# Optimization experiments

Measured on AMD Instinct MI355X. Metric: run time of the kernel, lower is better.

The kernel has to match this reference:

```python
import jax, jax.numpy as jnp
import numpy as np

B, H, E = 1024, 2048, 1024

def _xavier(key, shape):
    # torch xavier_normal_ on [1, out, in]: std = sqrt(2/(fan_in+fan_out)) over last two dims
    fan_out, fan_in = shape[-2], shape[-1]
    std = (2.0 / (fan_in + fan_out)) ** 0.5
    return jax.random.normal(key, shape, jnp.float32) * std

def setup_inputs() -> dict:
    key = jax.random.key(0)
    ks = jax.random.split(key, 17)
    inp = {
        'x': jax.random.normal(ks[0], (B, E, 1), jnp.float32),
        'c': jax.random.normal(ks[1], (B, H, 1), jnp.float32),
        'h': jax.random.normal(ks[2], (B, H, 1), jnp.float32),
        'W_xi': _xavier(ks[3], (1, H, E)), 'W_hi': _xavier(ks[4], (1, H, H)), 'B_i': _xavier(ks[5], (1, H, 1)),
        'W_xg': _xavier(ks[6], (1, H, E)), 'W_hg': _xavier(ks[7], (1, H, H)), 'B_g': _xavier(ks[8], (1, H, 1)),
        'W_xf': _xavier(ks[9], (1, H, E)), 'W_hf': _xavier(ks[10], (1, H, H)), 'B_f': _xavier(ks[11], (1, H, 1)),
        'W_xo': _xavier(ks[12], (1, H, E)), 'W_ho': _xavier(ks[13], (1, H, H)), 'B_o': _xavier(ks[14], (1, H, 1)),
        'W_hy': _xavier(ks[15], (1, E, H)), 'B_y': _xavier(ks[16], (1, E, 1)),
    }
    return inp

def reference(x, c, h, W_xi, W_hi, B_i, W_xg, W_hg, B_g, W_xf, W_hf, B_f, W_xo, W_ho, B_o, W_hy, B_y):
    # jnp.matmul broadcasts the leading batch dim: [1,H,E] @ [B,E,1] -> [B,H,1]
    i = jax.nn.sigmoid(jnp.matmul(W_xi, x) + jnp.matmul(W_hi, h) + B_i)
    g = jnp.tanh(jnp.matmul(W_xg, x) + jnp.matmul(W_hg, h) + B_g)
    f = jax.nn.sigmoid(jnp.matmul(W_xf, x) + jnp.matmul(W_hf, h) + B_f)
    c_new = f * c + i * g
    o = jax.nn.sigmoid(jnp.matmul(W_xo, x) + jnp.matmul(W_ho, h) + B_o)
    h_new = o * c_new  # NOTE: source uses o*c (no tanh), faithful to original
    y = jnp.tanh(jnp.matmul(W_hy, h_new) + B_y)
    return (y, c_new, h_new)
```

## Files before the change

### kernel.cpp

```cpp
#include <hip/hip_runtime.h>

#define B_SZ 1024
#define H_SZ 2048
#define E_SZ 1024

typedef float  f32x4 __attribute__((ext_vector_type(4)));
typedef short  s16x8 __attribute__((ext_vector_type(8)));

__device__ __forceinline__ unsigned short f2bf(float f) {
    unsigned u = __float_as_uint(f);
    u = u + 0x7fffu + ((u >> 16) & 1u);
    return (unsigned short)(u >> 16);
}
__device__ __forceinline__ float bf2f(unsigned short s) {
    return __uint_as_float(((unsigned)s) << 16);
}

struct CastArgs {
    const float*    src[11];
    unsigned short* dst[11];
    int             n[11];
};

__global__ __launch_bounds__(256) void cast_kernel(CastArgs a) {
    const int arr = blockIdx.y;
    const int n = a.n[arr];
    const float* __restrict__ s = a.src[arr];
    unsigned short* __restrict__ d = a.dst[arr];
    const int stride = gridDim.x * 256 * 4;
    for (int i = (blockIdx.x * 256 + threadIdx.x) * 4; i < n; i += stride) {
        float4 v = *(const float4*)(s + i);
        ushort4 o;
        o.x = f2bf(v.x); o.y = f2bf(v.y); o.z = f2bf(v.z); o.w = f2bf(v.w);
        *(ushort4*)(d + i) = o;
    }
}

__device__ __forceinline__ void gemm_accum(
    const unsigned short* __restrict__ A,
    const unsigned short* __restrict__ W,
    int K, int m0, int n0,
    unsigned short* lA, unsigned short* lB,
    f32x4 acc[4][4], int t)
{
    const int lane = t & 63;
    const int w    = t >> 6;
    const int wr   = (w >> 1) << 6;
    const int wc   = (w & 1) << 6;
    const int lr   = lane & 15;
    const int kq   = (lane >> 4) << 3;

    const int r0   = t >> 2;
    const int col0 = (t & 3) << 3;

    for (int k0 = 0; k0 < K; k0 += 32) {
        const unsigned short* ga0 = A + (size_t)(m0 + r0) * K + (k0 + col0);
        const unsigned short* ga1 = ga0 + (size_t)64 * K;
        const unsigned short* gb0 = W + (size_t)(n0 + r0) * K + (k0 + col0);
        const unsigned short* gb1 = gb0 + (size_t)64 * K;
        __builtin_amdgcn_global_load_lds(
            (const __attribute__((address_space(1))) unsigned int*)ga0,
            (__attribute__((address_space(3))) unsigned int*)(lA + t * 8), 16, 0, 0);
        __builtin_amdgcn_global_load_lds(
            (const __attribute__((address_space(1))) unsigned int*)ga1,
            (__attribute__((address_space(3))) unsigned int*)(lA + (t + 256) * 8), 16, 0, 0);
        __builtin_amdgcn_global_load_lds(
            (const __attribute__((address_space(1))) unsigned int*)gb0,
            (__attribute__((address_space(3))) unsigned int*)(lB + t * 8), 16, 0, 0);
        __builtin_amdgcn_global_load_lds(
            (const __attribute__((address_space(1))) unsigned int*)gb1,
            (__attribute__((address_space(3))) unsigned int*)(lB + (t + 256) * 8), 16, 0, 0);
        __syncthreads();

        s16x8 af[4], bfr[4];
#pragma unroll
        for (int i = 0; i < 4; ++i)
            af[i] = *(const s16x8*)(lA + (wr + i * 16 + lr) * 32 + kq);
#pragma unroll
        for (int j = 0; j < 4; ++j)
            bfr[j] = *(const s16x8*)(lB + (wc + j * 16 + lr) * 32 + kq);
#pragma unroll
        for (int i = 0; i < 4; ++i)
#pragma unroll
            for (int j = 0; j < 4; ++j)
                acc[i][j] = __builtin_amdgcn_mfma_f32_16x16x32_bf16(
                    af[i], bfr[j], acc[i][j], 0, 0, 0);
        __syncthreads();
    }
}

__global__ __launch_bounds__(256) void gates_kernel(
    const unsigned short* __restrict__ Xb,
    const unsigned short* __restrict__ Hb,
    const unsigned short* __restrict__ Wxb,
    const unsigned short* __restrict__ Whb,
    const float* __restrict__ bi, const float* __restrict__ bg,
    const float* __restrict__ bff, const float* __restrict__ bo,
    unsigned short* __restrict__ Z)
{
    __shared__ unsigned short lA[128 * 32];
    __shared__ unsigned short lB[128 * 32];
    const int t  = threadIdx.x;
    const int m0 = blockIdx.x * 128;
    const int q  = blockIdx.y >> 4;
    const int n0 = (blockIdx.y & 15) * 128;

    f32x4 acc[4][4] = {};
    gemm_accum(Xb, Wxb + (size_t)q * H_SZ * E_SZ, E_SZ, m0, n0, lA, lB, acc, t);
    gemm_accum(Hb, Whb + (size_t)q * H_SZ * H_SZ, H_SZ, m0, n0, lA, lB, acc, t);

    const float* bias = (q == 0) ? bi : (q == 1) ? bg : (q == 2) ? bff : bo;
    const int lane = t & 63, w = t >> 6;
    const int wr = (w >> 1) << 6, wc = (w & 1) << 6;
    const int lr = lane & 15, rq = (lane >> 4) << 2;
    unsigned short* Zq = Z + (size_t)q * B_SZ * H_SZ;
#pragma unroll
    for (int i = 0; i < 4; ++i) {
#pragma unroll
        for (int j = 0; j < 4; ++j) {
            const int n = n0 + wc + j * 16 + lr;
            const float bv = bias[n];
#pragma unroll
            for (int r = 0; r < 4; ++r) {
                const int m = m0 + wr + i * 16 + rq + r;
                const float v = acc[i][j][r] + bv;
                const float a = (q == 1) ? tanhf(v) : 1.0f / (1.0f + __expf(-v));
                Zq[(size_t)m * H_SZ + n] = f2bf(a);
            }
        }
    }
}

__global__ __launch_bounds__(256) void cell_kernel(
    const unsigned short* __restrict__ Z, const float* __restrict__ c,
    float* __restrict__ c_out, float* __restrict__ h_out,
    unsigned short* __restrict__ HnB)
{
    const size_t BH = (size_t)B_SZ * H_SZ;
    const int idx = (blockIdx.x * 256 + threadIdx.x) * 4;
    ushort4 iu = *(const ushort4*)(Z + idx);
    ushort4 gu = *(const ushort4*)(Z + BH + idx);
    ushort4 fu = *(const ushort4*)(Z + 2 * BH + idx);
    ushort4 ou = *(const ushort4*)(Z + 3 * BH + idx);
    float4 cv = *(const float4*)(c + idx);

    float cn[4], hn[4];
    cn[0] = bf2f(fu.x) * cv.x + bf2f(iu.x) * bf2f(gu.x);
    cn[1] = bf2f(fu.y) * cv.y + bf2f(iu.y) * bf2f(gu.y);
    cn[2] = bf2f(fu.z) * cv.z + bf2f(iu.z) * bf2f(gu.z);
    cn[3] = bf2f(fu.w) * cv.w + bf2f(iu.w) * bf2f(gu.w);
    hn[0] = bf2f(ou.x) * cn[0];
    hn[1] = bf2f(ou.y) * cn[1];
    hn[2] = bf2f(ou.z) * cn[2];
    hn[3] = bf2f(ou.w) * cn[3];

    *(float4*)(c_out + idx) = make_float4(cn[0], cn[1], cn[2], cn[3]);
    *(float4*)(h_out + idx) = make_float4(hn[0], hn[1], hn[2], hn[3]);
    ushort4 hb;
    hb.x = f2bf(hn[0]); hb.y = f2bf(hn[1]); hb.z = f2bf(hn[2]); hb.w = f2bf(hn[3]);
    *(ushort4*)(HnB + idx) = hb;
}

__global__ __launch_bounds__(256) void y_kernel(
    const unsigned short* __restrict__ Hn,
    const unsigned short* __restrict__ Wy,
    const float* __restrict__ by, float* __restrict__ yout)
{
    __shared__ unsigned short lA[128 * 32];
    __shared__ unsigned short lB[128 * 32];
    const int t  = threadIdx.x;
    const int m0 = blockIdx.x * 128;
    const int n0 = blockIdx.y * 128;

    f32x4 acc[4][4] = {};
    gemm_accum(Hn, Wy, H_SZ, m0, n0, lA, lB, acc, t);

    const int lane = t & 63, w = t >> 6;
    const int wr = (w >> 1) << 6, wc = (w & 1) << 6;
    const int lr = lane & 15, rq = (lane >> 4) << 2;
#pragma unroll
    for (int i = 0; i < 4; ++i) {
#pragma unroll
        for (int j = 0; j < 4; ++j) {
            const int n = n0 + wc + j * 16 + lr;
            const float bv = by[n];
#pragma unroll
            for (int r = 0; r < 4; ++r) {
                const int m = m0 + wr + i * 16 + rq + r;
                yout[(size_t)m * E_SZ + n] = tanhf(acc[i][j][r] + bv);
            }
        }
    }
}

extern "C" void kernel_launch(void* const* d_in, const int* in_sizes, int n_in,
                              void* d_out, int out_size, void* d_ws, size_t ws_size,
                              hipStream_t stream) {
    const float* x   = (const float*)d_in[0];
    const float* c   = (const float*)d_in[1];
    const float* h   = (const float*)d_in[2];
    const float* Wxi = (const float*)d_in[3];
    const float* Whi = (const float*)d_in[4];
    const float* Bi  = (const float*)d_in[5];
    const float* Wxg = (const float*)d_in[6];
    const float* Whg = (const float*)d_in[7];
    const float* Bg  = (const float*)d_in[8];
    const float* Wxf = (const float*)d_in[9];
    const float* Whf = (const float*)d_in[10];
    const float* Bf  = (const float*)d_in[11];
    const float* Wxo = (const float*)d_in[12];
    const float* Who = (const float*)d_in[13];
    const float* Bo  = (const float*)d_in[14];
    const float* Why = (const float*)d_in[15];
    const float* By  = (const float*)d_in[16];

    const size_t BE = (size_t)B_SZ * E_SZ, BH = (size_t)B_SZ * H_SZ;
    const size_t HE = (size_t)H_SZ * E_SZ, HH = (size_t)H_SZ * H_SZ;
    const size_t EH = (size_t)E_SZ * H_SZ;

    unsigned short* ws   = (unsigned short*)d_ws;
    unsigned short* Xb   = ws;
    unsigned short* Hb   = Xb + BE;
    unsigned short* Wxb  = Hb + BH;
    unsigned short* Whb  = Wxb + 4 * HE;
    unsigned short* Whyb = Whb + 4 * HH;
    unsigned short* Z    = Whyb + EH;
    unsigned short* HnB  = Z + 4 * BH;

    CastArgs ca;
    ca.src[0]  = x;   ca.dst[0]  = Xb;           ca.n[0]  = (int)BE;
    ca.src[1]  = h;   ca.dst[1]  = Hb;           ca.n[1]  = (int)BH;
    ca.src[2]  = Wxi; ca.dst[2]  = Wxb;          ca.n[2]  = (int)HE;
    ca.src[3]  = Wxg; ca.dst[3]  = Wxb + HE;     ca.n[3]  = (int)HE;
    ca.src[4]  = Wxf; ca.dst[4]  = Wxb + 2 * HE; ca.n[4]  = (int)HE;
    ca.src[5]  = Wxo; ca.dst[5]  = Wxb + 3 * HE; ca.n[5]  = (int)HE;
    ca.src[6]  = Whi; ca.dst[6]  = Whb;          ca.n[6]  = (int)HH;
    ca.src[7]  = Whg; ca.dst[7]  = Whb + HH;     ca.n[7]  = (int)HH;
    ca.src[8]  = Whf; ca.dst[8]  = Whb + 2 * HH; ca.n[8]  = (int)HH;
    ca.src[9]  = Who; ca.dst[9]  = Whb + 3 * HH; ca.n[9]  = (int)HH;
    ca.src[10] = Why; ca.dst[10] = Whyb;         ca.n[10] = (int)EH;

    hipLaunchKernelGGL(cast_kernel, dim3(1024, 11), dim3(256), 0, stream, ca);
    hipLaunchKernelGGL(gates_kernel, dim3(8, 64), dim3(256), 0, stream,
                       Xb, Hb, Wxb, Whb, Bi, Bg, Bf, Bo, Z);

    float* y_out = (float*)d_out;
    float* c_out = y_out + BE;
    float* h_out = c_out + BH;
    hipLaunchKernelGGL(cell_kernel, dim3((unsigned)(BH / 1024)), dim3(256), 0, stream,
                       Z, c, c_out, h_out, HnB);
    hipLaunchKernelGGL(y_kernel, dim3(8, 8), dim3(256), 0, stream,
                       HnB, Whyb, By, y_out);
}
```

Measured before the change: 309.2 us.

## Split-K the output GEMM and remap gate tiles for XCD-local weight reuse

The y GEMM was launched on only 64 blocks. It is now split four ways along K into 256 blocks that write fp32 partials into the reused Z buffer, and a separate reduce kernel sums the partials and applies bias and tanh. The gates kernel moves to a 1D grid whose block index is remapped so blocks on the same XCD share weight N-tiles, aiming for better L2 locality. The split adds an extra kernel launch and partial-sum traffic to memory.

```diff
diff --git a/kernel.cpp b/kernel.cpp
--- a/kernel.cpp
+++ b/kernel.cpp
@@ -39,7 +39,7 @@
 __device__ __forceinline__ void gemm_accum(
     const unsigned short* __restrict__ A,
     const unsigned short* __restrict__ W,
-    int K, int m0, int n0,
+    int ld, int kLen, int m0, int n0,
     unsigned short* lA, unsigned short* lB,
     f32x4 acc[4][4], int t)
 {
@@ -53,11 +53,11 @@
     const int r0   = t >> 2;
     const int col0 = (t & 3) << 3;
 
-    for (int k0 = 0; k0 < K; k0 += 32) {
-        const unsigned short* ga0 = A + (size_t)(m0 + r0) * K + (k0 + col0);
-        const unsigned short* ga1 = ga0 + (size_t)64 * K;
-        const unsigned short* gb0 = W + (size_t)(n0 + r0) * K + (k0 + col0);
-        const unsigned short* gb1 = gb0 + (size_t)64 * K;
+    for (int k0 = 0; k0 < kLen; k0 += 32) {
+        const unsigned short* ga0 = A + (size_t)(m0 + r0) * ld + (k0 + col0);
+        const unsigned short* ga1 = ga0 + (size_t)64 * ld;
+        const unsigned short* gb0 = W + (size_t)(n0 + r0) * ld + (k0 + col0);
+        const unsigned short* gb1 = gb0 + (size_t)64 * ld;
         __builtin_amdgcn_global_load_lds(
             (const __attribute__((address_space(1))) unsigned int*)ga0,
             (__attribute__((address_space(3))) unsigned int*)(lA + t * 8), 16, 0, 0);
@@ -100,14 +100,18 @@
 {
     __shared__ unsigned short lA[128 * 32];
     __shared__ unsigned short lB[128 * 32];
-    const int t  = threadIdx.x;
-    const int m0 = blockIdx.x * 128;
-    const int q  = blockIdx.y >> 4;
-    const int n0 = (blockIdx.y & 15) * 128;
+    const int t   = threadIdx.x;
+    const int b   = blockIdx.x;
+    const int xcd = b & 7;
+    const int i_  = b >> 3;
+    const int nt  = xcd * 8 + (i_ >> 3);
+    const int m0  = (i_ & 7) * 128;
+    const int q   = nt >> 4;
+    const int n0  = (nt & 15) * 128;
 
     f32x4 acc[4][4] = {};
-    gemm_accum(Xb, Wxb + (size_t)q * H_SZ * E_SZ, E_SZ, m0, n0, lA, lB, acc, t);
-    gemm_accum(Hb, Whb + (size_t)q * H_SZ * H_SZ, H_SZ, m0, n0, lA, lB, acc, t);
+    gemm_accum(Xb, Wxb + (size_t)q * H_SZ * E_SZ, E_SZ, E_SZ, m0, n0, lA, lB, acc, t);
+    gemm_accum(Hb, Whb + (size_t)q * H_SZ * H_SZ, H_SZ, H_SZ, m0, n0, lA, lB, acc, t);
 
     const float* bias = (q == 0) ? bi : (q == 1) ? bg : (q == 2) ? bff : bo;
     const int lane = t & 63, w = t >> 6;
@@ -161,36 +165,61 @@
     *(ushort4*)(HnB + idx) = hb;
 }
 
-__global__ __launch_bounds__(256) void y_kernel(
+__global__ __launch_bounds__(256) void y_split_kernel(
     const unsigned short* __restrict__ Hn,
     const unsigned short* __restrict__ Wy,
-    const float* __restrict__ by, float* __restrict__ yout)
+    float* __restrict__ part)
 {
     __shared__ unsigned short lA[128 * 32];
     __shared__ unsigned short lB[128 * 32];
-    const int t  = threadIdx.x;
-    const int m0 = blockIdx.x * 128;
-    const int n0 = blockIdx.y * 128;
+    const int t   = threadIdx.x;
+    const int b   = blockIdx.x;
+    const int xcd = b & 7;
+    const int i_  = b >> 3;
+    const int ns  = xcd * 4 + (i_ >> 3);
+    const int m0  = (i_ & 7) * 128;
+    const int n0  = (ns >> 2) * 128;
+    const int s   = ns & 3;
 
     f32x4 acc[4][4] = {};
-    gemm_accum(Hn, Wy, H_SZ, m0, n0, lA, lB, acc, t);
+    gemm_accum(Hn + s * 512, Wy + s * 512, H_SZ, 512, m0, n0, lA, lB, acc, t);
 
     const int lane = t & 63, w = t >> 6;
     const int wr = (w >> 1) << 6, wc = (w & 1) << 6;
     const int lr = lane & 15, rq = (lane >> 4) << 2;
+    float* P = part + (size_t)s * B_SZ * E_SZ;
 #pragma unroll
     for (int i = 0; i < 4; ++i) {
 #pragma unroll
         for (int j = 0; j < 4; ++j) {
             const int n = n0 + wc + j * 16 + lr;
-            const float bv = by[n];
 #pragma unroll
             for (int r = 0; r < 4; ++r) {
                 const int m = m0 + wr + i * 16 + rq + r;
-                yout[(size_t)m * E_SZ + n] = tanhf(acc[i][j][r] + bv);
+                P[(size_t)m * E_SZ + n] = acc[i][j][r];
             }
         }
     }
+}
+
+__global__ __launch_bounds__(256) void y_reduce_kernel(
+    const float* __restrict__ part, const float* __restrict__ by,
+    float* __restrict__ yout)
+{
+    const size_t BE = (size_t)B_SZ * E_SZ;
+    const int idx = (blockIdx.x * 256 + threadIdx.x) * 4;
+    float4 a = *(const float4*)(part + idx);
+    float4 b2 = *(const float4*)(part + BE + idx);
+    float4 c2 = *(const float4*)(part + 2 * BE + idx);
+    float4 d2 = *(const float4*)(part + 3 * BE + idx);
+    const int col = idx & (E_SZ - 1);
+    float4 bv = *(const float4*)(by + col);
+    float4 o;
+    o.x = tanhf(a.x + b2.x + c2.x + d2.x + bv.x);
+    o.y = tanhf(a.y + b2.y + c2.y + d2.y + bv.y);
+    o.z = tanhf(a.z + b2.z + c2.z + d2.z + bv.z);
+    o.w = tanhf(a.w + b2.w + c2.w + d2.w + bv.w);
+    *(float4*)(yout + idx) = o;
 }
 
 extern "C" void kernel_launch(void* const* d_in, const int* in_sizes, int n_in,
@@ -241,7 +270,7 @@
     ca.src[10] = Why; ca.dst[10] = Whyb;         ca.n[10] = (int)EH;
 
     hipLaunchKernelGGL(cast_kernel, dim3(1024, 11), dim3(256), 0, stream, ca);
-    hipLaunchKernelGGL(gates_kernel, dim3(8, 64), dim3(256), 0, stream,
+    hipLaunchKernelGGL(gates_kernel, dim3(512), dim3(256), 0, stream,
                        Xb, Hb, Wxb, Whb, Bi, Bg, Bf, Bo, Z);
 
     float* y_out = (float*)d_out;
@@ -249,6 +278,10 @@
     float* h_out = c_out + BH;
     hipLaunchKernelGGL(cell_kernel, dim3((unsigned)(BH / 1024)), dim3(256), 0, stream,
                        Z, c, c_out, h_out, HnB);
-    hipLaunchKernelGGL(y_kernel, dim3(8, 8), dim3(256), 0, stream,
-                       HnB, Whyb, By, y_out);
-}
+
+    float* part = (float*)Z;
+    hipLaunchKernelGGL(y_split_kernel, dim3(256), dim3(256), 0, stream,
+                       HnB, Whyb, part);
+    hipLaunchKernelGGL(y_reduce_kernel, dim3((unsigned)(BE / 1024)), dim3(256), 0, stream,
+                       part, By, y_out);
+}
```

New measurement: 281.2 us. 1.1x faster.
